# Kernel tuning notes

Measured on AMD Instinct MI355X. Metric: run time of the kernel, lower is better.

Reference implementation:

```python
import jax, jax.numpy as jnp
import numpy as np

EPSILON = 1e-15
LOG2 = 0.6931471805599453
N_VARS = 4096
BATCH = 512
OUT_SIZES = [16384, 8192, 4096, 2048]
FANINS = [4, 2, 4, 2]


def log1mexp(x):
    # accurate log(1 - exp(x)) for x < 0
    return jnp.where(x > -LOG2,
                     jnp.log(-jnp.expm1(x)),
                     jnp.log1p(-jnp.exp(x)))


def encode_input(pos):
    # rows: [-inf, 0, pos0, neg0, pos1, neg1, ...]
    neg = log1mexp(pos)
    inter = jnp.stack([pos, neg], axis=1).reshape(2 * pos.shape[0], pos.shape[1])
    head = jnp.stack([jnp.full(pos.shape[1:], -jnp.inf, pos.dtype),
                      jnp.zeros(pos.shape[1:], pos.dtype)])
    return jnp.concatenate([head, inter], axis=0)


def product_layer(x, ptrs, seg, n_out):
    return jax.ops.segment_sum(x[ptrs], seg, num_segments=n_out)


def sum_layer(x, ptrs, seg, n_out):
    g = x[ptrs]
    a = jax.lax.stop_gradient(jax.ops.segment_max(g, seg, num_segments=n_out))
    s = jax.ops.segment_sum(jnp.exp(g - a[seg]), seg, num_segments=n_out)
    return jnp.log(s + EPSILON) + a


def setup_inputs() -> dict:
    rng = np.random.default_rng(0)
    # log-probabilities in (-inf, 0): pos = log(u), u in (0,1)
    u = rng.uniform(1e-4, 1.0 - 1e-4, size=(N_VARS, BATCH)).astype(np.float32)
    x = jnp.asarray(np.log(u))

    inputs = {"x": x}
    prev_size = 2 * N_VARS + 2
    for i, (n_out, fanin) in enumerate(zip(OUT_SIZES, FANINS)):
        n_edges = n_out * fanin
        lo = 1 if i == 0 else 0  # avoid the -inf constant row at layer 0
        ptrs = rng.integers(lo, prev_size, size=n_edges).astype(np.int64)
        seg = np.repeat(np.arange(n_out, dtype=np.int64), fanin)
        inputs[f"ptrs{i}"] = jnp.asarray(ptrs)
        inputs[f"seg{i}"] = jnp.asarray(seg)
        prev_size = n_out
    return inputs


def reference(x, ptrs0, seg0, ptrs1, seg1, ptrs2, seg2, ptrs3, seg3):
    h = encode_input(x)
    ptrs = [ptrs0, ptrs1, ptrs2, ptrs3]
    segs = [seg0, seg1, seg2, seg3]
    for i, n_out in enumerate(OUT_SIZES):
        if i % 2 == 0:
            h = product_layer(h, ptrs[i], segs[i], n_out)
        else:
            h = sum_layer(h, ptrs[i], segs[i], n_out)
    return h
```

## Files before the change

### kernel.cpp

```cpp
#include <hip/hip_runtime.h>
#include <hip/hip_fp16.h>
#include <math.h>

#define BATCH    512
#define N_VARS   4096
#define H_ROWS   (2 * N_VARS + 2)
#define N_OUT1   8192
#define N_OUT3   2048
#define TPB      1024

#define S_U2       4100
#define ENC_BYTES  (S_U2 * 8)
#define ENC_WS_BYTES ((size_t)(BATCH / 2) * ENC_BYTES)
#define R1_BYTES   (N_OUT1 * 8)
#define SMEM_BYTES (ENC_BYTES + R1_BYTES)

__device__ __forceinline__ float log1mexp_fast(float x) {
    return __logf(1.0f - __expf(x));
}

__device__ __forceinline__ float2 lse2_fast2(float2 a, float2 b) {
    float2 r;
    r.x = fmaxf(a.x, b.x) + __logf(1.0f + __expf(-fabsf(a.x - b.x)));
    r.y = fmaxf(a.y, b.y) + __logf(1.0f + __expf(-fabsf(a.y - b.y)));
    return r;
}

__device__ __forceinline__ unsigned int h2u(__half2 h) {
    union { __half2 h; unsigned int u; } v; v.h = h; return v.u;
}

__device__ __forceinline__ float2 gsum_h(const __half2* __restrict__ enc, int4 q) {
    __half2 v0 = enc[q.x], v1 = enc[q.y], v2 = enc[q.z], v3 = enc[q.w];
    __half2 s01 = __hadd2(v0, v1), s23 = __hadd2(v2, v3);
    float2 f01 = __half22float2(s01), f23 = __half22float2(s23);
    return make_float2(f01.x + f23.x, f01.y + f23.y);
}

__device__ __forceinline__ float2 gsum_f(const float2* __restrict__ rb, int4 q) {
    float2 v0 = rb[q.x], v1 = rb[q.y], v2 = rb[q.z], v3 = rb[q.w];
    return make_float2(v0.x + v1.x + v2.x + v3.x, v0.y + v1.y + v2.y + v3.y);
}

#define TDIM    32
#define NTRANS  ((BATCH / TDIM) * (N_VARS / TDIM))
#define NTAB    ((N_OUT1 + N_OUT3) / 256)
__global__ void prep_kernel(const float* __restrict__ x,
                            uint2* __restrict__ encE,
                            const int* __restrict__ p0,
                            const int* __restrict__ p1,
                            const int* __restrict__ p2,
                            const int* __restrict__ p3,
                            int4* __restrict__ tabB,
                            int4* __restrict__ tabC) {
    __shared__ float tile[TDIM][TDIM + 1];
    int blk = blockIdx.x;
    int tx = threadIdx.x, ty = threadIdx.y;
    if (blk < NTRANS) {
        int cb = (blk % (BATCH / TDIM)) * TDIM;
        int rb = (blk / (BATCH / TDIM)) * TDIM;
#pragma unroll
        for (int j = 0; j < TDIM; j += 8)
            tile[ty + j][tx] = x[(size_t)(rb + ty + j) * BATCH + cb + tx];
        __syncthreads();
        int tid = ty * TDIM + tx;
#pragma unroll
        for (int k = 0; k < 2; ++k) {
            int q = tid + k * 256;
            int vl = q & 31;
            int pl = q >> 5;
            float a = tile[vl][2 * pl];
            float b = tile[vl][2 * pl + 1];
            uint2 val;
            val.x = h2u(__floats2half2_rn(a, b));
            val.y = h2u(__floats2half2_rn(log1mexp_fast(a), log1mexp_fast(b)));
            encE[(size_t)(cb / 2 + pl) * S_U2 + 1 + rb + vl] = val;
        }
        if (rb == 0 && tid < 16)
            encE[(size_t)(cb / 2 + tid) * S_U2] = make_uint2(0xFC00FC00u, 0u);
    } else {
        int o = (blk - NTRANS) * 256 + ty * TDIM + tx;
        if (o < N_OUT1) {
            int2 pp = ((const int2*)p1)[o];
            tabB[2 * o]     = ((const int4*)p0)[pp.x];
            tabB[2 * o + 1] = ((const int4*)p0)[pp.y];
        } else {
            int oc = o - N_OUT1;
            int2 pp = ((const int2*)p3)[oc];
            tabC[2 * oc]     = ((const int4*)p2)[pp.x];
            tabC[2 * oc + 1] = ((const int4*)p2)[pp.y];
        }
    }
}

__global__ void __launch_bounds__(TPB, 4)
fused_spn_kernel(const uint2* __restrict__ encE,
                 const int4* __restrict__ tabB,
                 const int4* __restrict__ tabC,
                 float* __restrict__ out) {
    extern __shared__ char smem[];
    const __half2* enc = (const __half2*)smem;
    float2* r1b = (float2*)(smem + ENC_BYTES);
    const int bp = blockIdx.x;
    const int t  = threadIdx.x;

    const uint2* src = encE + (size_t)bp * S_U2;
    uint2 e0 = src[t], e1 = src[t + 1024], e2 = src[t + 2048], e3 = src[t + 3072];
    int4 a0A = tabB[2 * t],          b0A = tabB[2 * t + 1];
    int4 a1A = tabB[2 * (t + 1024)], b1A = tabB[2 * (t + 1024) + 1];
    {
        uint2* lu2 = (uint2*)smem;
        lu2[t] = e0; lu2[t + 1024] = e1; lu2[t + 2048] = e2; lu2[t + 3072] = e3;
        if (t == 0) lu2[4096] = src[4096];
    }
    __syncthreads();

    int4 a0B = tabB[2 * (t + 2048)], b0B = tabB[2 * (t + 2048) + 1];
    int4 a1B = tabB[2 * (t + 3072)], b1B = tabB[2 * (t + 3072) + 1];
    r1b[t]        = lse2_fast2(gsum_h(enc, a0A), gsum_h(enc, b0A));
    r1b[t + 1024] = lse2_fast2(gsum_h(enc, a1A), gsum_h(enc, b1A));
    a0A = tabB[2 * (t + 4096)]; b0A = tabB[2 * (t + 4096) + 1];
    a1A = tabB[2 * (t + 5120)]; b1A = tabB[2 * (t + 5120) + 1];
    r1b[t + 2048] = lse2_fast2(gsum_h(enc, a0B), gsum_h(enc, b0B));
    r1b[t + 3072] = lse2_fast2(gsum_h(enc, a1B), gsum_h(enc, b1B));
    a0B = tabB[2 * (t + 6144)]; b0B = tabB[2 * (t + 6144) + 1];
    a1B = tabB[2 * (t + 7168)]; b1B = tabB[2 * (t + 7168) + 1];
    r1b[t + 4096] = lse2_fast2(gsum_h(enc, a0A), gsum_h(enc, b0A));
    r1b[t + 5120] = lse2_fast2(gsum_h(enc, a1A), gsum_h(enc, b1A));
    int4 ca0 = tabC[2 * t],          cb0 = tabC[2 * t + 1];
    int4 ca1 = tabC[2 * (t + 1024)], cb1 = tabC[2 * (t + 1024) + 1];
    r1b[t + 6144] = lse2_fast2(gsum_h(enc, a0B), gsum_h(enc, b0B));
    r1b[t + 7168] = lse2_fast2(gsum_h(enc, a1B), gsum_h(enc, b1B));
    __syncthreads();

    {
        float2 ga = gsum_f(r1b, ca0), gb = gsum_f(r1b, cb0);
        ((float2*)(out + (size_t)t * BATCH))[bp] = lse2_fast2(ga, gb);
        float2 ga1 = gsum_f(r1b, ca1), gb1 = gsum_f(r1b, cb1);
        ((float2*)(out + (size_t)(t + 1024) * BATCH))[bp] = lse2_fast2(ga1, gb1);
    }
}

extern "C" void kernel_launch(void* const* d_in, const int* in_sizes, int n_in,
                              void* d_out, int out_size, void* d_ws, size_t ws_size,
                              hipStream_t stream) {
    const float* x     = (const float*)d_in[0];
    const int*   ptrs0 = (const int*)d_in[1];
    const int*   ptrs1 = (const int*)d_in[3];
    const int*   ptrs2 = (const int*)d_in[5];
    const int*   ptrs3 = (const int*)d_in[7];
    float* out = (float*)d_out;

    uint2* encE = (uint2*)d_ws;
    int4*  tabB = (int4*)((char*)d_ws + ENC_WS_BYTES);
    int4*  tabC = tabB + 2 * N_OUT1;

    hipFuncSetAttribute((const void*)fused_spn_kernel,
                        hipFuncAttributeMaxDynamicSharedMemorySize, SMEM_BYTES);

    prep_kernel<<<NTRANS + NTAB, dim3(32, 8), 0, stream>>>(
        x, encE, ptrs0, ptrs1, ptrs2, ptrs3, tabB, tabC);

    fused_spn_kernel<<<BATCH / 2, TPB, SMEM_BYTES, stream>>>(encE, tabB, tabC, out);
}
```

Baseline: 88.81 us.

## Fuse input encoding and pointer composition into single SPN kernel

Removes the separate prep kernel that transposed and encoded x into a workspace and built composed pointer tables. The main kernel now reads x directly with strided float2 loads per batch pair, encodes into LDS, and resolves the two-level pointer indirection (p1->p0, p3->p2) inline, interleaved with compute. Block index is swizzled so neighbouring blocks touch different column groups. This saves a launch and a workspace round trip, but the x reads are now strided, uncoalesced 8-byte accesses, and every block repeats the pointer composition.

```diff
diff --git a/kernel.cpp b/kernel.cpp
--- a/kernel.cpp
+++ b/kernel.cpp
@@ -4,14 +4,12 @@
 
 #define BATCH    512
 #define N_VARS   4096
-#define H_ROWS   (2 * N_VARS + 2)
+#define H_DW     8194
 #define N_OUT1   8192
 #define N_OUT3   2048
 #define TPB      1024
 
-#define S_U2       4100
-#define ENC_BYTES  (S_U2 * 8)
-#define ENC_WS_BYTES ((size_t)(BATCH / 2) * ENC_BYTES)
+#define ENC_BYTES  32800
 #define R1_BYTES   (N_OUT1 * 8)
 #define SMEM_BYTES (ENC_BYTES + R1_BYTES)
 
@@ -30,6 +28,13 @@
     union { __half2 h; unsigned int u; } v; v.h = h; return v.u;
 }
 
+__device__ __forceinline__ uint2 enc2(float2 v) {
+    uint2 r;
+    r.x = h2u(__floats2half2_rn(v.x, v.y));
+    r.y = h2u(__floats2half2_rn(log1mexp_fast(v.x), log1mexp_fast(v.y)));
+    return r;
+}
+
 __device__ __forceinline__ float2 gsum_h(const __half2* __restrict__ enc, int4 q) {
     __half2 v0 = enc[q.x], v1 = enc[q.y], v2 = enc[q.z], v3 = enc[q.w];
     __half2 s01 = __hadd2(v0, v1), s23 = __hadd2(v2, v3);
@@ -42,101 +47,77 @@
     return make_float2(v0.x + v1.x + v2.x + v3.x, v0.y + v1.y + v2.y + v3.y);
 }
 
-#define TDIM    32
-#define NTRANS  ((BATCH / TDIM) * (N_VARS / TDIM))
-#define NTAB    ((N_OUT1 + N_OUT3) / 256)
-__global__ void prep_kernel(const float* __restrict__ x,
-                            uint2* __restrict__ encE,
-                            const int* __restrict__ p0,
-                            const int* __restrict__ p1,
-                            const int* __restrict__ p2,
-                            const int* __restrict__ p3,
-                            int4* __restrict__ tabB,
-                            int4* __restrict__ tabC) {
-    __shared__ float tile[TDIM][TDIM + 1];
-    int blk = blockIdx.x;
-    int tx = threadIdx.x, ty = threadIdx.y;
-    if (blk < NTRANS) {
-        int cb = (blk % (BATCH / TDIM)) * TDIM;
-        int rb = (blk / (BATCH / TDIM)) * TDIM;
-#pragma unroll
-        for (int j = 0; j < TDIM; j += 8)
-            tile[ty + j][tx] = x[(size_t)(rb + ty + j) * BATCH + cb + tx];
-        __syncthreads();
-        int tid = ty * TDIM + tx;
-#pragma unroll
-        for (int k = 0; k < 2; ++k) {
-            int q = tid + k * 256;
-            int vl = q & 31;
-            int pl = q >> 5;
-            float a = tile[vl][2 * pl];
-            float b = tile[vl][2 * pl + 1];
-            uint2 val;
-            val.x = h2u(__floats2half2_rn(a, b));
-            val.y = h2u(__floats2half2_rn(log1mexp_fast(a), log1mexp_fast(b)));
-            encE[(size_t)(cb / 2 + pl) * S_U2 + 1 + rb + vl] = val;
-        }
-        if (rb == 0 && tid < 16)
-            encE[(size_t)(cb / 2 + tid) * S_U2] = make_uint2(0xFC00FC00u, 0u);
-    } else {
-        int o = (blk - NTRANS) * 256 + ty * TDIM + tx;
-        if (o < N_OUT1) {
-            int2 pp = ((const int2*)p1)[o];
-            tabB[2 * o]     = ((const int4*)p0)[pp.x];
-            tabB[2 * o + 1] = ((const int4*)p0)[pp.y];
-        } else {
-            int oc = o - N_OUT1;
-            int2 pp = ((const int2*)p3)[oc];
-            tabC[2 * oc]     = ((const int4*)p2)[pp.x];
-            tabC[2 * oc + 1] = ((const int4*)p2)[pp.y];
-        }
-    }
-}
-
 __global__ void __launch_bounds__(TPB, 4)
-fused_spn_kernel(const uint2* __restrict__ encE,
-                 const int4* __restrict__ tabB,
-                 const int4* __restrict__ tabC,
-                 float* __restrict__ out) {
+spn_one_kernel(const float* __restrict__ x,
+               const int* __restrict__ p0,
+               const int* __restrict__ p1,
+               const int* __restrict__ p2,
+               const int* __restrict__ p3,
+               float* __restrict__ out) {
     extern __shared__ char smem[];
     const __half2* enc = (const __half2*)smem;
     float2* r1b = (float2*)(smem + ENC_BYTES);
-    const int bp = blockIdx.x;
+    const int b  = blockIdx.x;
+    const int bp = ((b & 7) << 5) | (b >> 3);
     const int t  = threadIdx.x;
 
-    const uint2* src = encE + (size_t)bp * S_U2;
-    uint2 e0 = src[t], e1 = src[t + 1024], e2 = src[t + 2048], e3 = src[t + 3072];
-    int4 a0A = tabB[2 * t],          b0A = tabB[2 * t + 1];
-    int4 a1A = tabB[2 * (t + 1024)], b1A = tabB[2 * (t + 1024) + 1];
+    const int2* P1 = (const int2*)p1;
+    const int4* P0 = (const int4*)p0;
+    const int2* P3 = (const int2*)p3;
+    const int4* P2 = (const int4*)p2;
+
+    const float2* xc = (const float2*)x + bp;
+    float2 v0 = xc[(size_t)t * (BATCH / 2)];
+    float2 v1 = xc[((size_t)t + 1024) * (BATCH / 2)];
+    float2 v2 = xc[((size_t)t + 2048) * (BATCH / 2)];
+    float2 v3 = xc[((size_t)t + 3072) * (BATCH / 2)];
+
+    int2 i0 = P1[t], i1 = P1[t + 1024], i2 = P1[t + 2048], i3 = P1[t + 3072];
+
     {
         uint2* lu2 = (uint2*)smem;
-        lu2[t] = e0; lu2[t + 1024] = e1; lu2[t + 2048] = e2; lu2[t + 3072] = e3;
-        if (t == 0) lu2[4096] = src[4096];
+        if (t == 0) lu2[0] = make_uint2(0xFC00FC00u, 0u);
+        lu2[1 + t]        = enc2(v0);
+        lu2[1 + t + 1024] = enc2(v1);
+        lu2[1 + t + 2048] = enc2(v2);
+        lu2[1 + t + 3072] = enc2(v3);
     }
+    int4 a0 = P0[i0.x], b0 = P0[i0.y];
+    int4 a1 = P0[i1.x], b1 = P0[i1.y];
     __syncthreads();
 
-    int4 a0B = tabB[2 * (t + 2048)], b0B = tabB[2 * (t + 2048) + 1];
-    int4 a1B = tabB[2 * (t + 3072)], b1B = tabB[2 * (t + 3072) + 1];
-    r1b[t]        = lse2_fast2(gsum_h(enc, a0A), gsum_h(enc, b0A));
-    r1b[t + 1024] = lse2_fast2(gsum_h(enc, a1A), gsum_h(enc, b1A));
-    a0A = tabB[2 * (t + 4096)]; b0A = tabB[2 * (t + 4096) + 1];
-    a1A = tabB[2 * (t + 5120)]; b1A = tabB[2 * (t + 5120) + 1];
-    r1b[t + 2048] = lse2_fast2(gsum_h(enc, a0B), gsum_h(enc, b0B));
-    r1b[t + 3072] = lse2_fast2(gsum_h(enc, a1B), gsum_h(enc, b1B));
-    a0B = tabB[2 * (t + 6144)]; b0B = tabB[2 * (t + 6144) + 1];
-    a1B = tabB[2 * (t + 7168)]; b1B = tabB[2 * (t + 7168) + 1];
-    r1b[t + 4096] = lse2_fast2(gsum_h(enc, a0A), gsum_h(enc, b0A));
-    r1b[t + 5120] = lse2_fast2(gsum_h(enc, a1A), gsum_h(enc, b1A));
-    int4 ca0 = tabC[2 * t],          cb0 = tabC[2 * t + 1];
-    int4 ca1 = tabC[2 * (t + 1024)], cb1 = tabC[2 * (t + 1024) + 1];
-    r1b[t + 6144] = lse2_fast2(gsum_h(enc, a0B), gsum_h(enc, b0B));
-    r1b[t + 7168] = lse2_fast2(gsum_h(enc, a1B), gsum_h(enc, b1B));
+    int4 a2 = P0[i2.x], b2 = P0[i2.y];
+    int4 a3 = P0[i3.x], b3 = P0[i3.y];
+    int2 i4 = P1[t + 4096], i5 = P1[t + 5120];
+    int2 i6 = P1[t + 6144], i7 = P1[t + 7168];
+
+    r1b[t]        = lse2_fast2(gsum_h(enc, a0), gsum_h(enc, b0));
+    r1b[t + 1024] = lse2_fast2(gsum_h(enc, a1), gsum_h(enc, b1));
+
+    int4 a4 = P0[i4.x], b4 = P0[i4.y];
+    int4 a5 = P0[i5.x], b5 = P0[i5.y];
+
+    r1b[t + 2048] = lse2_fast2(gsum_h(enc, a2), gsum_h(enc, b2));
+    r1b[t + 3072] = lse2_fast2(gsum_h(enc, a3), gsum_h(enc, b3));
+
+    int4 a6 = P0[i6.x], b6 = P0[i6.y];
+    int4 a7 = P0[i7.x], b7 = P0[i7.y];
+    int2 c0i = P3[t], c1i = P3[t + 1024];
+
+    r1b[t + 4096] = lse2_fast2(gsum_h(enc, a4), gsum_h(enc, b4));
+    r1b[t + 5120] = lse2_fast2(gsum_h(enc, a5), gsum_h(enc, b5));
+
+    int4 ca = P2[c0i.x], cb = P2[c0i.y];
+    int4 cc = P2[c1i.x], cd = P2[c1i.y];
+
+    r1b[t + 6144] = lse2_fast2(gsum_h(enc, a6), gsum_h(enc, b6));
+    r1b[t + 7168] = lse2_fast2(gsum_h(enc, a7), gsum_h(enc, b7));
     __syncthreads();
 
     {
-        float2 ga = gsum_f(r1b, ca0), gb = gsum_f(r1b, cb0);
+        float2 ga = gsum_f(r1b, ca), gb = gsum_f(r1b, cb);
         ((float2*)(out + (size_t)t * BATCH))[bp] = lse2_fast2(ga, gb);
-        float2 ga1 = gsum_f(r1b, ca1), gb1 = gsum_f(r1b, cb1);
+        float2 ga1 = gsum_f(r1b, cc), gb1 = gsum_f(r1b, cd);
         ((float2*)(out + (size_t)(t + 1024) * BATCH))[bp] = lse2_fast2(ga1, gb1);
     }
 }
@@ -150,16 +131,11 @@
     const int*   ptrs2 = (const int*)d_in[5];
     const int*   ptrs3 = (const int*)d_in[7];
     float* out = (float*)d_out;
+    (void)d_ws; (void)ws_size;
 
-    uint2* encE = (uint2*)d_ws;
-    int4*  tabB = (int4*)((char*)d_ws + ENC_WS_BYTES);
-    int4*  tabC = tabB + 2 * N_OUT1;
-
-    hipFuncSetAttribute((const void*)fused_spn_kernel,
+    hipFuncSetAttribute((const void*)spn_one_kernel,
                         hipFuncAttributeMaxDynamicSharedMemorySize, SMEM_BYTES);
 
-    prep_kernel<<<NTRANS + NTAB, dim3(32, 8), 0, stream>>>(
-        x, encE, ptrs0, ptrs1, ptrs2, ptrs3, tabB, tabC);
-
-    fused_spn_kernel<<<BATCH / 2, TPB, SMEM_BYTES, stream>>>(encE, tabB, tabC, out);
+    spn_one_kernel<<<BATCH / 2, TPB, SMEM_BYTES, stream>>>(
+        x, ptrs0, ptrs1, ptrs2, ptrs3, out);
 }
```

After: 98.18 us. 10.6% more time.
